# Performance work log

Measured on AMD Instinct MI355X. Metric: run time of the kernel, lower is better.

Reference implementation:

```python
import jax, jax.numpy as jnp
import numpy as np

ENT_TYPE_SIZE = 9
INNER_DIM = 64
NEG_INF = 1e12


def _rope_interleaved(x, cos_pos, sin_pos):
    # x: (B, S, H, D); rotate interleaved pairs: (x0,x1)->(x0*c - x1*s, x1*c + x0*s)
    x2 = jnp.stack([-x[..., 1::2], x[..., ::2]], axis=-1).reshape(x.shape)
    return x * cos_pos + x2 * sin_pos


def setup_inputs() -> dict:
    key = jax.random.key(0)
    k1, k2 = jax.random.split(key)
    B, S, H = 16, 512, 768
    out_dim = ENT_TYPE_SIZE * INNER_DIM * 2  # 1152
    last_hidden_state = jax.random.normal(k1, (B, S, H), dtype=jnp.float32)
    attention_mask = jnp.ones((B, S), dtype=jnp.float32)
    W_dense = jax.random.normal(k2, (H, out_dim), dtype=jnp.float32) * (1.0 / np.sqrt(H))
    b_dense = jnp.zeros((out_dim,), dtype=jnp.float32)
    return {
        "last_hidden_state": last_hidden_state,
        "attention_mask": attention_mask,
        "W_dense": W_dense,
        "b_dense": b_dense,
    }


def reference(last_hidden_state, attention_mask, W_dense, b_dense):
    B, S, H = last_hidden_state.shape
    ent, inner = ENT_TYPE_SIZE, INNER_DIM

    # dense projection then split into per-entity-type q/k vectors
    proj = last_hidden_state @ W_dense + b_dense            # (B, S, ent*2*inner)
    proj = proj.reshape(B, S, ent, 2 * inner)
    qw, kw = proj[..., :inner], proj[..., inner:]           # (B, S, ent, inner)

    # inline RoPE, interleaved sin/cos layout per sinusoidal_position_embedding
    pos = jnp.arange(S, dtype=jnp.float32)[:, None]         # (S, 1)
    idx = jnp.arange(inner // 2, dtype=jnp.float32)
    freqs = pos * jnp.power(10000.0, -2.0 * idx / inner)    # (S, inner/2)
    cos_pos = jnp.repeat(jnp.cos(freqs), 2, axis=-1)[None, :, None, :]  # (1,S,1,inner)
    sin_pos = jnp.repeat(jnp.sin(freqs), 2, axis=-1)[None, :, None, :]
    qw = _rope_interleaved(qw, cos_pos, sin_pos)
    kw = _rope_interleaved(kw, cos_pos, sin_pos)

    # pairwise span scores
    logits = jnp.einsum('bmhd,bnhd->bhmn', qw, kw)          # (B, ent, S, S)

    # padding mask on key positions (canonical GlobalPointer masking)
    pad = attention_mask[:, None, None, :]                  # (B,1,1,S)
    logits = logits * pad - (1.0 - pad) * NEG_INF

    # strict lower triangle masked out (only spans with start <= end)
    tril = jnp.tril(jnp.ones((S, S), dtype=logits.dtype), -1)
    logits = logits - tril * NEG_INF

    return logits / (inner ** 0.5)
```

## Files before the change

### kernel.cpp

```cpp
#include <hip/hip_runtime.h>
#include <hip/hip_bf16.h>
#include <cstdint>

typedef __bf16 bf8 __attribute__((ext_vector_type(8)));
typedef __bf16 bf4 __attribute__((ext_vector_type(4)));
typedef float  f4  __attribute__((ext_vector_type(4)));

typedef const void __attribute__((address_space(1)))* as1_cvp;
typedef void       __attribute__((address_space(3)))* as3_vp;

#define NEG_INF_F 1000000000000.0f

__device__ __forceinline__ void lds_load16(const __bf16* g, __bf16* l) {
    __builtin_amdgcn_global_load_lds((as1_cvp)g, (as3_vp)l, 16, 0, 0);
}

__device__ __forceinline__ void gemm_tile_core_swapped(
    const __bf16* __restrict__ Atile, const __bf16* __restrict__ Btile,
    int lda, int ldb, int Ktot,
    __bf16* sA, __bf16* sB, f4 acc[4][4])
{
    const int t    = threadIdx.x;
    const int wave = t >> 6;
    const int lane = t & 63;
    const int quad = lane >> 4;
    const int m16  = lane & 15;
    const int wm   = (wave >> 1) * 64;
    const int wn   = (wave & 1) * 64;

    const int f0   = t;
    const int row0 = f0 >> 2;
    const int ch0  = (f0 & 3) * 8;
    const int f1   = 256 + t;
    const int row1 = f1 >> 2;
    const int ch1  = (f1 & 3) * 8;
    const int l0   = (wave * 64) * 8;
    const int l1   = (256 + wave * 64) * 8;

    lds_load16(Atile + (size_t)row0 * lda + ch0, sA + l0);
    lds_load16(Btile + (size_t)row0 * ldb + ch0, sB + l0);
    lds_load16(Atile + (size_t)row1 * lda + ch1, sA + l1);
    lds_load16(Btile + (size_t)row1 * ldb + ch1, sB + l1);
    __syncthreads();

    const int nIter = Ktot >> 5;
    for (int k = 0; k < nIter; ++k) {
        const int cur = (k & 1) * 4096;
        if (k + 1 < nIter) {
            const int nxt = ((k + 1) & 1) * 4096;
            const int k0n = (k + 1) << 5;
            lds_load16(Atile + (size_t)row0 * lda + k0n + ch0, sA + nxt + l0);
            lds_load16(Btile + (size_t)row0 * ldb + k0n + ch0, sB + nxt + l0);
            lds_load16(Atile + (size_t)row1 * lda + k0n + ch1, sA + nxt + l1);
            lds_load16(Btile + (size_t)row1 * ldb + k0n + ch1, sB + nxt + l1);
        }

        bf8 af[4], bfr[4];
#pragma unroll
        for (int mi = 0; mi < 4; ++mi)
            af[mi] = *(const bf8*)(sA + cur + (wm + mi * 16 + m16) * 32 + quad * 8);
#pragma unroll
        for (int ni = 0; ni < 4; ++ni)
            bfr[ni] = *(const bf8*)(sB + cur + (wn + ni * 16 + m16) * 32 + quad * 8);
#pragma unroll
        for (int mi = 0; mi < 4; ++mi)
#pragma unroll
            for (int ni = 0; ni < 4; ++ni)
                acc[mi][ni] = __builtin_amdgcn_mfma_f32_16x16x32_bf16(
                    bfr[ni], af[mi], acc[mi][ni], 0, 0, 0);

        __syncthreads();
    }
}

__global__ __launch_bounds__(256) void prep_kernel(
    const float* __restrict__ lhs, __bf16* __restrict__ Abf,
    const float* __restrict__ W,   __bf16* __restrict__ Wt)
{
    __shared__ __bf16 tile[32][33];
    const int t  = threadIdx.x;
    int bx = blockIdx.x;
    if (bx < 6144) {
        const int idx = bx * 256 + t;
        const float4 v = reinterpret_cast<const float4*>(lhs)[idx];
        bf4 o = { (__bf16)v.x, (__bf16)v.y, (__bf16)v.z, (__bf16)v.w };
        reinterpret_cast<bf4*>(Abf)[idx] = o;
    } else {
        bx -= 6144;
        const int n0 = (bx % 36) * 32;
        const int k0 = (bx / 36) * 32;
        const int tx = t & 31;
        const int ty = t >> 5;
#pragma unroll
        for (int r = 0; r < 32; r += 8)
            tile[ty + r][tx] = (__bf16)W[(size_t)(k0 + ty + r) * 1152 + n0 + tx];
        __syncthreads();
#pragma unroll
        for (int r = 0; r < 32; r += 8)
            Wt[(size_t)(n0 + ty + r) * 768 + k0 + tx] = tile[tx][ty + r];
    }
}

__global__ __launch_bounds__(256) void proj_rope_kernel(
    const __bf16* __restrict__ A,
    const __bf16* __restrict__ Wt,
    const float*  __restrict__ bias,
    __bf16* __restrict__ qbuf, __bf16* __restrict__ kbuf)
{
    __shared__ __bf16 sA[2 * 128 * 32];
    __shared__ __bf16 sB[2 * 128 * 32];
    f4 acc[4][4] = {};

    const int rowTile = blockIdx.y * 128;
    const int colTile = blockIdx.x * 128;
    gemm_tile_core_swapped(A + (size_t)rowTile * 768, Wt + (size_t)colTile * 768,
                           768, 768, 768, sA, sB, acc);

    const int t = threadIdx.x, wave = t >> 6, lane = t & 63;
    const int quad = lane >> 4, m16 = lane & 15;
    const int wm = (wave >> 1) * 64, wn = (wave & 1) * 64;

#pragma unroll
    for (int ni = 0; ni < 4; ++ni) {
        const int gc0 = colTile + wn + ni * 16 + quad * 4;
        const int e   = gc0 >> 7;
        const int d0  = gc0 & 63;
        const int qk  = (gc0 >> 6) & 1;
        const float4 bv = *reinterpret_cast<const float4*>(bias + gc0);
        const float th0 = exp2f((float)(d0 >> 1)       * -0.4152410118609203f);
        const float th1 = exp2f((float)((d0 >> 1) + 1) * -0.4152410118609203f);
        __bf16* base = (qk ? kbuf : qbuf);
#pragma unroll
        for (int mi = 0; mi < 4; ++mi) {
            const int gm = rowTile + wm + mi * 16 + m16;
            const int bb = gm >> 9;
            const int s  = gm & 511;
            const float sf = (float)s;
            float v0 = acc[mi][ni][0] + bv.x;
            float v1 = acc[mi][ni][1] + bv.y;
            float v2 = acc[mi][ni][2] + bv.z;
            float v3 = acc[mi][ni][3] + bv.w;
            float sn0, cs0, sn1, cs1;
            __sincosf(sf * th0, &sn0, &cs0);
            __sincosf(sf * th1, &sn1, &cs1);
            bf4 o = { (__bf16)(v0 * cs0 - v1 * sn0),
                      (__bf16)(v1 * cs0 + v0 * sn0),
                      (__bf16)(v2 * cs1 - v3 * sn1),
                      (__bf16)(v3 * cs1 + v2 * sn1) };
            *reinterpret_cast<bf4*>(
                base + ((size_t)((bb * 9 + e) * 512 + s)) * 64 + d0) = o;
        }
    }
}

__global__ __launch_bounds__(256, 3) void logits_kernel(
    const __bf16* __restrict__ qbuf, const __bf16* __restrict__ kbuf,
    const float* __restrict__ amask, float* __restrict__ out)
{
    const int t    = threadIdx.x;
    const int wave = t >> 6;
    const int lane = t & 63;
    const int quad = lane >> 4;
    const int m16  = lane & 15;
    const int wm   = (wave >> 1) * 64;
    const int ncol = (wave & 1) * 256;

    const int be = blockIdx.y;
    const int b  = be / 9;
    const int rowTile = blockIdx.x * 128;
    const int rowbase = rowTile + wm;

    int c0 = (rowbase - ncol) >> 6;
    c0 = c0 < 0 ? 0 : (c0 > 4 ? 4 : c0);

    const __bf16* Qg = qbuf + (size_t)be * 512 * 64 + (size_t)rowbase * 64;
    const __bf16* Kg = kbuf + (size_t)be * 512 * 64;

    bf8 af[2][4];
#pragma unroll
    for (int kp = 0; kp < 2; ++kp)
#pragma unroll
        for (int mi = 0; mi < 4; ++mi)
            af[kp][mi] = *reinterpret_cast<const bf8*>(
                Qg + (mi * 16 + m16) * 64 + kp * 32 + quad * 8);

    const float* amr  = amask + b * 512;
    float*       outw = out + ((size_t)(be * 512 + rowbase) << 9);

#pragma unroll
    for (int c = 0; c < 4; ++c) {
        const int n0 = ncol + c * 64;
        if (c >= c0) {
            const __bf16* Kc = Kg + (size_t)n0 * 64;
            bf8 bfr[2][4];
#pragma unroll
            for (int kp = 0; kp < 2; ++kp)
#pragma unroll
                for (int ni = 0; ni < 4; ++ni)
                    bfr[kp][ni] = *reinterpret_cast<const bf8*>(
                        Kc + (ni * 16 + m16) * 64 + kp * 32 + quad * 8);

            f4 acc[4][4] = {};
#pragma unroll
            for (int kp = 0; kp < 2; ++kp)
#pragma unroll
                for (int mi = 0; mi < 4; ++mi)
#pragma unroll
                    for (int ni = 0; ni < 4; ++ni)
                        acc[mi][ni] = __builtin_amdgcn_mfma_f32_16x16x32_bf16(
                            bfr[kp][ni], af[kp][mi], acc[mi][ni], 0, 0, 0);

#pragma unroll
            for (int ni = 0; ni < 4; ++ni) {
                const int nq = n0 + ni * 16 + quad * 4;
                const float4 pv = *reinterpret_cast<const float4*>(amr + nq);
                const float pp[4] = { pv.x, pv.y, pv.z, pv.w };
#pragma unroll
                for (int mi = 0; mi < 4; ++mi) {
                    const int m = rowbase + mi * 16 + m16;
                    const f4 a = acc[mi][ni];
                    float4 res;
                    float* rp = &res.x;
#pragma unroll
                    for (int r = 0; r < 4; ++r) {
                        float v = a[r] * pp[r] - (1.0f - pp[r]) * NEG_INF_F;
                        if (nq + r < m) v -= NEG_INF_F;
                        rp[r] = v * 0.125f;
                    }
                    *reinterpret_cast<float4*>(
                        outw + (((size_t)(mi * 16 + m16)) << 9) + nq) = res;
                }
            }
        } else {
#pragma unroll
            for (int ni = 0; ni < 4; ++ni) {
                const int nq = n0 + ni * 16 + quad * 4;
                const float4 pv = *reinterpret_cast<const float4*>(amr + nq);
                const float pp[4] = { pv.x, pv.y, pv.z, pv.w };
                float4 res;
                float* rp = &res.x;
#pragma unroll
                for (int r = 0; r < 4; ++r)
                    rp[r] = (-(1.0f - pp[r]) * NEG_INF_F - NEG_INF_F) * 0.125f;
#pragma unroll
                for (int mi = 0; mi < 4; ++mi)
                    *reinterpret_cast<float4*>(
                        outw + (((size_t)(mi * 16 + m16)) << 9) + nq) = res;
            }
        }
    }
}

extern "C" void kernel_launch(void* const* d_in, const int* in_sizes, int n_in,
                              void* d_out, int out_size, void* d_ws, size_t ws_size,
                              hipStream_t stream) {
    const float* lhs   = (const float*)d_in[0];
    const float* amask = (const float*)d_in[1];
    const float* W     = (const float*)d_in[2];
    const float* bias  = (const float*)d_in[3];
    float* out = (float*)d_out;

    char* ws = (char*)d_ws;
    __bf16* Abf = (__bf16*)ws;
    __bf16* Wt  = (__bf16*)(ws + 12582912);
    __bf16* qb  = (__bf16*)(ws + 14352384);
    __bf16* kb  = (__bf16*)(ws + 23789568);

    prep_kernel<<<7008, 256, 0, stream>>>(lhs, Abf, W, Wt);
    proj_rope_kernel<<<dim3(9, 64), 256, 0, stream>>>(Abf, Wt, bias, qb, kb);
    logits_kernel<<<dim3(4, 144), 256, 0, stream>>>(qb, kb, amask, out);
}
```

Baseline: 229.9 us.

## Fuse fp32-to-bf16 activation conversion into projection GEMM A-tile loads

Removes the separate pass that converted the 16x512x768 fp32 hidden state to bf16 in a workspace. The GEMM now loads fp32 A tiles into registers, converts them and writes bf16 to LDS after the MFMAs, while W still uses direct global-to-LDS loads. The grid is also flattened with a block-index swizzle that spreads tiles across XCDs for L2 locality. This cuts a full read and write of the activations, but the GEMM now reads twice the A bytes and adds VGPR pressure and conversion ALU work in the main loop.

```diff
diff --git a/kernel.cpp b/kernel.cpp
--- a/kernel.cpp
+++ b/kernel.cpp
@@ -15,11 +15,41 @@
     __builtin_amdgcn_global_load_lds((as1_cvp)g, (as3_vp)l, 16, 0, 0);
 }
 
-__device__ __forceinline__ void gemm_tile_core_swapped(
-    const __bf16* __restrict__ Atile, const __bf16* __restrict__ Btile,
-    int lda, int ldb, int Ktot,
-    __bf16* sA, __bf16* sB, f4 acc[4][4])
+__global__ __launch_bounds__(256) void transpose_w_kernel(
+    const float* __restrict__ W, __bf16* __restrict__ Wt)
 {
+    __shared__ __bf16 tile[32][33];
+    const int n0 = blockIdx.x * 32;
+    const int k0 = blockIdx.y * 32;
+    const int tx = threadIdx.x & 31;
+    const int ty = threadIdx.x >> 5;
+#pragma unroll
+    for (int r = 0; r < 32; r += 8)
+        tile[ty + r][tx] = (__bf16)W[(size_t)(k0 + ty + r) * 1152 + n0 + tx];
+    __syncthreads();
+#pragma unroll
+    for (int r = 0; r < 32; r += 8)
+        Wt[(size_t)(n0 + ty + r) * 768 + k0 + tx] = tile[tx][ty + r];
+}
+
+__global__ __launch_bounds__(256) void proj_rope_kernel(
+    const float*  __restrict__ A,
+    const __bf16* __restrict__ Wt,
+    const float*  __restrict__ bias,
+    __bf16* __restrict__ qbuf, __bf16* __restrict__ kbuf)
+{
+    __shared__ __bf16 sA[2 * 128 * 32];
+    __shared__ __bf16 sB[2 * 128 * 32];
+    f4 acc[4][4] = {};
+
+    const int bid = blockIdx.x;
+    const int wid = (bid & 7) * 72 + (bid >> 3);
+    const int rowTile = (wid / 9) * 128;
+    const int colTile = (wid % 9) * 128;
+
+    const float*  Ag = A  + (size_t)rowTile * 768;
+    const __bf16* Bg = Wt + (size_t)colTile * 768;
+
     const int t    = threadIdx.x;
     const int wave = t >> 6;
     const int lane = t & 63;
@@ -28,31 +58,42 @@
     const int wm   = (wave >> 1) * 64;
     const int wn   = (wave & 1) * 64;
 
-    const int f0   = t;
-    const int row0 = f0 >> 2;
-    const int ch0  = (f0 & 3) * 8;
-    const int f1   = 256 + t;
-    const int row1 = f1 >> 2;
-    const int ch1  = (f1 & 3) * 8;
-    const int l0   = (wave * 64) * 8;
-    const int l1   = (256 + wave * 64) * 8;
-
-    lds_load16(Atile + (size_t)row0 * lda + ch0, sA + l0);
-    lds_load16(Btile + (size_t)row0 * ldb + ch0, sB + l0);
-    lds_load16(Atile + (size_t)row1 * lda + ch1, sA + l1);
-    lds_load16(Btile + (size_t)row1 * ldb + ch1, sB + l1);
+    const int f0 = t,       row0 = f0 >> 2, k80 = (f0 & 3) * 8;
+    const int f1 = t + 256, row1 = f1 >> 2, k81 = (f1 & 3) * 8;
+    const int lb0 = (wave * 64) * 8;
+    const int lb1 = (256 + wave * 64) * 8;
+
+    {
+        const float4 a00 = *(const float4*)(Ag + (size_t)row0 * 768 + k80);
+        const float4 a01 = *(const float4*)(Ag + (size_t)row0 * 768 + k80 + 4);
+        const float4 a10 = *(const float4*)(Ag + (size_t)row1 * 768 + k81);
+        const float4 a11 = *(const float4*)(Ag + (size_t)row1 * 768 + k81 + 4);
+        lds_load16(Bg + (size_t)row0 * 768 + k80, sB + lb0);
+        lds_load16(Bg + (size_t)row1 * 768 + k81, sB + lb1);
+        bf8 w0 = { (__bf16)a00.x, (__bf16)a00.y, (__bf16)a00.z, (__bf16)a00.w,
+                   (__bf16)a01.x, (__bf16)a01.y, (__bf16)a01.z, (__bf16)a01.w };
+        bf8 w1 = { (__bf16)a10.x, (__bf16)a10.y, (__bf16)a10.z, (__bf16)a10.w,
+                   (__bf16)a11.x, (__bf16)a11.y, (__bf16)a11.z, (__bf16)a11.w };
+        *(bf8*)(sA + f0 * 8) = w0;
+        *(bf8*)(sA + f1 * 8) = w1;
+    }
     __syncthreads();
 
-    const int nIter = Ktot >> 5;
+    const int nIter = 24;
     for (int k = 0; k < nIter; ++k) {
         const int cur = (k & 1) * 4096;
-        if (k + 1 < nIter) {
-            const int nxt = ((k + 1) & 1) * 4096;
-            const int k0n = (k + 1) << 5;
-            lds_load16(Atile + (size_t)row0 * lda + k0n + ch0, sA + nxt + l0);
-            lds_load16(Btile + (size_t)row0 * ldb + k0n + ch0, sB + nxt + l0);
-            lds_load16(Atile + (size_t)row1 * lda + k0n + ch1, sA + nxt + l1);
-            lds_load16(Btile + (size_t)row1 * ldb + k0n + ch1, sB + nxt + l1);
+        const int nxt = ((k + 1) & 1) * 4096;
+
+        float4 a00, a01, a10, a11;
+        const bool pf = (k + 1 < nIter);
+        if (pf) {
+            const int kn = (k + 1) << 5;
+            a00 = *(const float4*)(Ag + (size_t)row0 * 768 + kn + k80);
+            a01 = *(const float4*)(Ag + (size_t)row0 * 768 + kn + k80 + 4);
+            a10 = *(const float4*)(Ag + (size_t)row1 * 768 + kn + k81);
+            a11 = *(const float4*)(Ag + (size_t)row1 * 768 + kn + k81 + 4);
+            lds_load16(Bg + (size_t)row0 * 768 + kn + k80, sB + nxt + lb0);
+            lds_load16(Bg + (size_t)row1 * 768 + kn + k81, sB + nxt + lb1);
         }
 
         bf8 af[4], bfr[4];
@@ -69,56 +110,16 @@
                 acc[mi][ni] = __builtin_amdgcn_mfma_f32_16x16x32_bf16(
                     bfr[ni], af[mi], acc[mi][ni], 0, 0, 0);
 
+        if (pf) {
+            bf8 w0 = { (__bf16)a00.x, (__bf16)a00.y, (__bf16)a00.z, (__bf16)a00.w,
+                       (__bf16)a01.x, (__bf16)a01.y, (__bf16)a01.z, (__bf16)a01.w };
+            bf8 w1 = { (__bf16)a10.x, (__bf16)a10.y, (__bf16)a10.z, (__bf16)a10.w,
+                       (__bf16)a11.x, (__bf16)a11.y, (__bf16)a11.z, (__bf16)a11.w };
+            *(bf8*)(sA + nxt + f0 * 8) = w0;
+            *(bf8*)(sA + nxt + f1 * 8) = w1;
+        }
         __syncthreads();
     }
-}
-
-__global__ __launch_bounds__(256) void prep_kernel(
-    const float* __restrict__ lhs, __bf16* __restrict__ Abf,
-    const float* __restrict__ W,   __bf16* __restrict__ Wt)
-{
-    __shared__ __bf16 tile[32][33];
-    const int t  = threadIdx.x;
-    int bx = blockIdx.x;
-    if (bx < 6144) {
-        const int idx = bx * 256 + t;
-        const float4 v = reinterpret_cast<const float4*>(lhs)[idx];
-        bf4 o = { (__bf16)v.x, (__bf16)v.y, (__bf16)v.z, (__bf16)v.w };
-        reinterpret_cast<bf4*>(Abf)[idx] = o;
-    } else {
-        bx -= 6144;
-        const int n0 = (bx % 36) * 32;
-        const int k0 = (bx / 36) * 32;
-        const int tx = t & 31;
-        const int ty = t >> 5;
-#pragma unroll
-        for (int r = 0; r < 32; r += 8)
-            tile[ty + r][tx] = (__bf16)W[(size_t)(k0 + ty + r) * 1152 + n0 + tx];
-        __syncthreads();
-#pragma unroll
-        for (int r = 0; r < 32; r += 8)
-            Wt[(size_t)(n0 + ty + r) * 768 + k0 + tx] = tile[tx][ty + r];
-    }
-}
-
-__global__ __launch_bounds__(256) void proj_rope_kernel(
-    const __bf16* __restrict__ A,
-    const __bf16* __restrict__ Wt,
-    const float*  __restrict__ bias,
-    __bf16* __restrict__ qbuf, __bf16* __restrict__ kbuf)
-{
-    __shared__ __bf16 sA[2 * 128 * 32];
-    __shared__ __bf16 sB[2 * 128 * 32];
-    f4 acc[4][4] = {};
-
-    const int rowTile = blockIdx.y * 128;
-    const int colTile = blockIdx.x * 128;
-    gemm_tile_core_swapped(A + (size_t)rowTile * 768, Wt + (size_t)colTile * 768,
-                           768, 768, 768, sA, sB, acc);
-
-    const int t = threadIdx.x, wave = t >> 6, lane = t & 63;
-    const int quad = lane >> 4, m16 = lane & 15;
-    const int wm = (wave >> 1) * 64, wn = (wave & 1) * 64;
 
 #pragma unroll
     for (int ni = 0; ni < 4; ++ni) {
@@ -261,12 +262,11 @@
     float* out = (float*)d_out;
 
     char* ws = (char*)d_ws;
-    __bf16* Abf = (__bf16*)ws;
-    __bf16* Wt  = (__bf16*)(ws + 12582912);
-    __bf16* qb  = (__bf16*)(ws + 14352384);
-    __bf16* kb  = (__bf16*)(ws + 23789568);
-
-    prep_kernel<<<7008, 256, 0, stream>>>(lhs, Abf, W, Wt);
-    proj_rope_kernel<<<dim3(9, 64), 256, 0, stream>>>(Abf, Wt, bias, qb, kb);
+    __bf16* Wt = (__bf16*)ws;
+    __bf16* qb = (__bf16*)(ws + 1769472);
+    __bf16* kb = (__bf16*)(ws + 11206656);
+
+    transpose_w_kernel<<<dim3(36, 24), 256, 0, stream>>>(W, Wt);
+    proj_rope_kernel<<<576, 256, 0, stream>>>(lhs, Wt, bias, qb, kb);
     logits_kernel<<<dim3(4, 144), 256, 0, stream>>>(qb, kb, amask, out);
 }
```

Result: no change. 229.6 us (-0.1%).
